# Optimization experiments

Hardware: AMD Instinct MI355X
Metric: run time of the kernel (lower is better)

Reference implementation:

```python
import jax, jax.numpy as jnp
import numpy as np

B = 2
L = 1024
D_MODEL = 1024
D_INNER = 2048   # expand * d_model
D_STATE = 16
DT_RANK = 64     # ceil(d_model / 16)
D_CONV = 4


def setup_inputs() -> dict:
    key = jax.random.key(0)
    ks = jax.random.split(key, 8)
    def nrm(k, shape, scale):
        return jax.random.normal(k, shape, dtype=jnp.float32) * scale
    A_log = jnp.log(jnp.tile(jnp.arange(1, D_STATE + 1, dtype=jnp.float32)[None, :], (D_INNER, 1)))
    return dict(
        hidden_states=jax.random.normal(ks[0], (B, L, D_MODEL), dtype=jnp.float32),
        Win=nrm(ks[1], (D_MODEL, 2 * D_INNER), D_MODEL ** -0.5),
        Wx=nrm(ks[2], (D_INNER, DT_RANK + 2 * D_STATE), D_INNER ** -0.5),
        Wdt=nrm(ks[3], (DT_RANK, D_INNER), DT_RANK ** -0.5),
        dt_bias=nrm(ks[4], (D_INNER,), 1.0),
        Wout=nrm(ks[5], (D_INNER, D_MODEL), D_INNER ** -0.5),
        dw_kernel=nrm(ks[6], (D_CONV, D_INNER), 0.2),
        dw_bias=jnp.zeros((D_INNER,), dtype=jnp.float32),
        A_log=A_log,
        Dskip=jnp.ones((D_INNER,), dtype=jnp.float32),
    )


def _causal_depthwise_conv(x, kernel, bias):
    # x: (B, L, D_INNER), kernel: (k, D_INNER); dilation 1, causal left pad
    k = kernel.shape[0]
    Lq = x.shape[1]
    xpad = jnp.pad(x, ((0, 0), (k - 1, 0), (0, 0)))
    y = sum(xpad[:, i:i + Lq, :] * kernel[i] for i in range(k)) + bias
    return jax.nn.silu(y)


def _selective_scan(u, delta, A, Bm, Cm, Dskip, z):
    # u, delta, z: (B, L, D); A: (D, N); Bm, Cm: (B, L, N)
    deltaA = jnp.exp(jnp.einsum('bld,dn->bldn', delta, A))      # (B,L,D,N)
    deltaBu = jnp.einsum('bld,bln,bld->bldn', delta, Bm, u)     # (B,L,D,N)

    def step(x_prev, elems):
        dA, dBu, c = elems                                      # (B,D,N),(B,D,N),(B,N)
        x_new = dA * x_prev + dBu
        y = jnp.einsum('bdn,bn->bd', x_new, c)
        return x_new, y

    x0 = jnp.zeros((u.shape[0], u.shape[2], A.shape[1]), dtype=jnp.float32)
    _, ys = jax.lax.scan(
        step, x0,
        (deltaA.transpose(1, 0, 2, 3), deltaBu.transpose(1, 0, 2, 3), Cm.transpose(1, 0, 2)))
    y = ys.transpose(1, 0, 2) + u * Dskip                        # skip connection
    return y * jax.nn.silu(z)


def reference(hidden_states, Win, Wx, Wdt, dt_bias, Wout, dw_kernel, dw_bias, A_log, Dskip):
    xz = hidden_states @ Win                                     # (B,L,2*D_INNER)
    x, z = jnp.split(xz, 2, axis=-1)
    A = -jnp.exp(A_log)                                          # (D_INNER, D_STATE)
    x = _causal_depthwise_conv(x, dw_kernel, dw_bias)
    x_dbl = x @ Wx                                               # (B,L,DT_RANK+2*N)
    dt, Bm, Cm = jnp.split(x_dbl, [DT_RANK, DT_RANK + D_STATE], axis=-1)
    delta = jax.nn.softplus(dt @ Wdt + dt_bias)                  # delta_bias + softplus
    y = _selective_scan(x, delta, A, Bm, Cm, Dskip, z)
    return y @ Wout
```

## Files before the change

kernel.cpp:

```cpp
#include <hip/hip_runtime.h>
#include <hip/hip_bf16.h>
#include <math.h>

#define B_SZ 2
#define L_SZ 1024
#define DM 1024
#define DI 2048
#define NS 16
#define DTR 64
#define NCHUNK 16
#define CLEN 64
#define XDLD 128
#define KSPLIT 8

typedef unsigned short ushortT;
typedef __attribute__((ext_vector_type(8))) short short8;
typedef __attribute__((ext_vector_type(4))) float floatx4;

__device__ __forceinline__ ushortT f2bf(float f) {
  unsigned u = __float_as_uint(f);
  unsigned r = (u + 0x7fff + ((u >> 16) & 1)) >> 16;
  return (ushortT)r;
}

__device__ __forceinline__ void gl2lds16(const void* g, void* l) {
  __builtin_amdgcn_global_load_lds(
      (const __attribute__((address_space(1))) unsigned int*)g,
      (__attribute__((address_space(3))) unsigned int*)l, 16, 0, 0);
}

__device__ __forceinline__ unsigned stash_addr(unsigned i) {
  return (i >> 10) * 4096 + 1024 + (i & 1023);
}

__global__ __launch_bounds__(256) void cvt_bf16(const float* __restrict__ src,
                                                ushortT* __restrict__ dst) {
  const int i = blockIdx.x * 256 + threadIdx.x;
  float4 v = ((const float4*)src)[i];
  unsigned lo = (unsigned)f2bf(v.x) | ((unsigned)f2bf(v.y) << 16);
  unsigned hi = (unsigned)f2bf(v.z) | ((unsigned)f2bf(v.w) << 16);
  ((uint2*)dst)[i] = make_uint2(lo, hi);
}

__global__ __launch_bounds__(256) void transpose_bf16(
    const float* __restrict__ src, ushortT* __restrict__ dst, int R, int C) {
  __shared__ float t[32][33];
  const int bx = blockIdx.x * 32;
  const int by = blockIdx.y * 32;
  const int tx = threadIdx.x, ty = threadIdx.y;
#pragma unroll
  for (int j = 0; j < 4; ++j)
    t[ty + j * 8][tx] = src[(size_t)(by + ty + j * 8) * C + bx + tx];
  __syncthreads();
#pragma unroll
  for (int j = 0; j < 4; ++j)
    dst[(size_t)(bx + ty + j * 8) * R + by + tx] = f2bf(t[tx][ty + j * 8]);
}

__global__ __launch_bounds__(256) void wx_pad_t(const float* __restrict__ Wx,
                                                ushortT* __restrict__ WxT) {
  const int k = blockIdx.x * 256 + threadIdx.x;
  const int n = blockIdx.y;
  WxT[(size_t)n * DI + k] = (n < 96) ? f2bf(Wx[(size_t)k * 96 + n]) : (ushortT)0;
}

__global__ __launch_bounds__(128) void gemm1_bk64(
    const ushortT* __restrict__ A, int lda,
    const ushortT* __restrict__ BT, int ldb,
    float* __restrict__ C, int ldc, int K) {
  __shared__ __align__(16) char smem[128 * 128 + 64 * 128];
  char* As = smem;
  char* Bs = smem + 128 * 128;
  const int tid = threadIdx.x;
  const int lane = tid & 63;
  const int quad = lane >> 4;
  const int l16 = lane & 15;
  const int wm = tid >> 6;
  const int m0 = blockIdx.y * 128;
  const int n0 = blockIdx.x * 64;

  floatx4 acc[4][4] = {};

  for (int k0 = 0; k0 < K; k0 += 64) {
    for (int i = tid; i < 128 * 8; i += 128) {
      const int r = i >> 3, c = i & 7;
      const int cg = c ^ (r & 7);
      gl2lds16(A + (size_t)(m0 + r) * lda + k0 + cg * 8, As + (i - lane) * 16);
    }
    for (int i = tid; i < 64 * 8; i += 128) {
      const int r = i >> 3, c = i & 7;
      const int cg = c ^ (r & 7);
      gl2lds16(BT + (size_t)(n0 + r) * ldb + k0 + cg * 8, Bs + (i - lane) * 16);
    }
    __syncthreads();

    short8 afr[4][2], bfr[4][2];
#pragma unroll
    for (int i = 0; i < 4; ++i) {
      const int r = wm * 64 + i * 16 + l16;
#pragma unroll
      for (int s = 0; s < 2; ++s)
        afr[i][s] = *(const short8*)(As + r * 128 + (((s * 4 + quad) ^ (r & 7)) * 16));
    }
#pragma unroll
    for (int j = 0; j < 4; ++j) {
      const int r = j * 16 + l16;
#pragma unroll
      for (int s = 0; s < 2; ++s)
        bfr[j][s] = *(const short8*)(Bs + r * 128 + (((s * 4 + quad) ^ (r & 7)) * 16));
    }
#pragma unroll
    for (int s = 0; s < 2; ++s)
#pragma unroll
      for (int i = 0; i < 4; ++i)
#pragma unroll
        for (int j = 0; j < 4; ++j)
          acc[i][j] = __builtin_amdgcn_mfma_f32_16x16x32_bf16(afr[i][s], bfr[j][s],
                                                              acc[i][j], 0, 0, 0);
    __syncthreads();
  }
#pragma unroll
  for (int i = 0; i < 4; ++i)
#pragma unroll
    for (int j = 0; j < 4; ++j)
#pragma unroll
      for (int r = 0; r < 4; ++r) {
        const int m = m0 + wm * 64 + i * 16 + quad * 4 + r;
        const int n = n0 + j * 16 + l16;
        C[(size_t)m * ldc + n] = acc[i][j][r];
      }
}

__global__ __launch_bounds__(128) void gemm_out_split(
    const ushortT* __restrict__ A, int lda,
    const ushortT* __restrict__ BT, int ldb,
    float* __restrict__ part) {
  __shared__ __align__(16) char smem[64 * 128 + 64 * 128];
  char* As = smem;
  char* Bs = smem + 64 * 128;
  const int tid = threadIdx.x;
  const int lane = tid & 63;
  const int quad = lane >> 4;
  const int l16 = lane & 15;
  const int wm = tid >> 6;
  const int m0 = blockIdx.y * 64;
  const int n0 = blockIdx.x * 64;
  const int kb = blockIdx.z * (DI / 2);

  floatx4 acc[2][4] = {};

  for (int k0 = kb; k0 < kb + DI / 2; k0 += 64) {
    for (int i = tid; i < 64 * 8; i += 128) {
      const int r = i >> 3, c = i & 7;
      const int cg = c ^ (r & 7);
      gl2lds16(A + (size_t)(m0 + r) * lda + k0 + cg * 8, As + (i - lane) * 16);
    }
    for (int i = tid; i < 64 * 8; i += 128) {
      const int r = i >> 3, c = i & 7;
      const int cg = c ^ (r & 7);
      gl2lds16(BT + (size_t)(n0 + r) * ldb + k0 + cg * 8, Bs + (i - lane) * 16);
    }
    __syncthreads();

    short8 afr[2][2], bfr[4][2];
#pragma unroll
    for (int i = 0; i < 2; ++i) {
      const int m = wm * 32 + i * 16 + l16;
#pragma unroll
      for (int s = 0; s < 2; ++s)
        afr[i][s] = *(const short8*)(As + m * 128 + (((s * 4 + quad) ^ (m & 7)) * 16));
    }
#pragma unroll
    for (int j = 0; j < 4; ++j) {
      const int n = j * 16 + l16;
#pragma unroll
      for (int s = 0; s < 2; ++s)
        bfr[j][s] = *(const short8*)(Bs + n * 128 + (((s * 4 + quad) ^ (n & 7)) * 16));
    }
#pragma unroll
    for (int s = 0; s < 2; ++s)
#pragma unroll
      for (int i = 0; i < 2; ++i)
#pragma unroll
        for (int j = 0; j < 4; ++j)
          acc[i][j] = __builtin_amdgcn_mfma_f32_16x16x32_bf16(afr[i][s], bfr[j][s],
                                                              acc[i][j], 0, 0, 0);
    __syncthreads();
  }
  float* out = part + (size_t)blockIdx.z * (B_SZ * L_SZ * DM);
#pragma unroll
  for (int i = 0; i < 2; ++i)
#pragma unroll
    for (int j = 0; j < 4; ++j)
#pragma unroll
      for (int r = 0; r < 4; ++r) {
        const int m = m0 + wm * 32 + i * 16 + quad * 4 + r;
        const int n = n0 + j * 16 + l16;
        out[(size_t)m * DM + n] = acc[i][j][r];
      }
}

__global__ __launch_bounds__(256) void reduce_out(const float* __restrict__ part,
                                                  float* __restrict__ out) {
  const int i = blockIdx.x * 256 + threadIdx.x;
  const float4 a = ((const float4*)part)[i];
  const float4 b = ((const float4*)part)[(size_t)(B_SZ * L_SZ * DM / 4) + i];
  ((float4*)out)[i] = make_float4(a.x + b.x, a.y + b.y, a.z + b.z, a.w + b.w);
}

__global__ __launch_bounds__(256) void gemm_xdbl_mfma(
    const float* __restrict__ xc, const ushortT* __restrict__ WxT,
    float* __restrict__ part) {
  __shared__ __align__(16) char smem[64 * 128 + 128 * 64];
  char* As = smem;
  char* Bs = smem + 64 * 128;
  const int tid = threadIdx.x;
  const int lane = tid & 63;
  const int quad = lane >> 4;
  const int l16 = lane & 15;
  const int wid = tid >> 6;
  const int wm = wid & 1;
  const int wn = wid >> 1;
  const int m0 = blockIdx.x * 64;
  const int kbase = blockIdx.y * (DI / KSPLIT);

  floatx4 acc[2][4] = {};

  for (int kk = 0; kk < DI / KSPLIT; kk += 32) {
    const int k0 = kbase + kk;
    for (int i = tid; i < 64 * 8; i += 256) {
      const int r = i >> 3, c = i & 7;
      const int cg = c ^ (r & 7);
      gl2lds16(xc + (size_t)(m0 + r) * DI + k0 + cg * 4, As + (i - lane) * 16);
    }
    for (int i = tid; i < 128 * 4; i += 256) {
      const int r = i >> 2, c = i & 3;
      const int cg = c ^ (r & 3);
      gl2lds16(WxT + (size_t)r * DI + k0 + cg * 8, Bs + (i - lane) * 16);
    }
    __syncthreads();

    short8 afr[2], bfr[4];
#pragma unroll
    for (int i = 0; i < 2; ++i) {
      const int m = wm * 32 + i * 16 + l16;
      const float4 x0 = *(const float4*)(As + m * 128 + (((quad * 2 + 0) ^ (m & 7)) * 16));
      const float4 x1 = *(const float4*)(As + m * 128 + (((quad * 2 + 1) ^ (m & 7)) * 16));
      short8 f;
      f[0] = (short)f2bf(x0.x); f[1] = (short)f2bf(x0.y);
      f[2] = (short)f2bf(x0.z); f[3] = (short)f2bf(x0.w);
      f[4] = (short)f2bf(x1.x); f[5] = (short)f2bf(x1.y);
      f[6] = (short)f2bf(x1.z); f[7] = (short)f2bf(x1.w);
      afr[i] = f;
    }
#pragma unroll
    for (int j = 0; j < 4; ++j) {
      const int n = wn * 64 + j * 16 + l16;
      bfr[j] = *(const short8*)(Bs + n * 64 + ((quad ^ (n & 3)) * 16));
    }
#pragma unroll
    for (int i = 0; i < 2; ++i)
#pragma unroll
      for (int j = 0; j < 4; ++j)
        acc[i][j] = __builtin_amdgcn_mfma_f32_16x16x32_bf16(afr[i], bfr[j],
                                                            acc[i][j], 0, 0, 0);
    __syncthreads();
  }
  float* out = part + (size_t)blockIdx.y * (B_SZ * L_SZ * XDLD);
#pragma unroll
  for (int i = 0; i < 2; ++i)
#pragma unroll
    for (int j = 0; j < 4; ++j)
#pragma unroll
      for (int r = 0; r < 4; ++r) {
        const int m = m0 + wm * 32 + i * 16 + quad * 4 + r;
        const int n = wn * 64 + j * 16 + l16;
        out[(size_t)m * XDLD + n] = acc[i][j][r];
      }
}

__global__ __launch_bounds__(256) void xdbl_reduce(const float* __restrict__ part,
                                                   float* __restrict__ xdbl) {
  const int i = blockIdx.x * 256 + threadIdx.x;
  float4 a = ((const float4*)part)[i];
#pragma unroll
  for (int s = 1; s < KSPLIT; ++s) {
    const float4 b = ((const float4*)part)[(size_t)s * (B_SZ * L_SZ * XDLD / 4) + i];
    a.x += b.x; a.y += b.y; a.z += b.z; a.w += b.w;
  }
  ((float4*)xdbl)[i] = a;
}

__global__ __launch_bounds__(256) void conv_silu(
    const float* __restrict__ xz, const float* __restrict__ kern,
    const float* __restrict__ bias, float* __restrict__ xc) {
  const int d = blockIdx.y * 256 + threadIdx.x;
  const int b = blockIdx.x >> 7;
  const int l0 = (blockIdx.x & 127) * 8;
  const int row0 = b * L_SZ + l0;
  const float k0v = kern[0 * DI + d], k1v = kern[1 * DI + d];
  const float k2v = kern[2 * DI + d], k3v = kern[3 * DI + d];
  float xv[11];
#pragma unroll
  for (int i = 0; i < 11; ++i) {
    const int l = l0 - 3 + i;
    xv[i] = (l >= 0) ? xz[((size_t)(b * L_SZ + l)) * 4096 + d] : 0.f;
  }
  const float bs = bias[d];
#pragma unroll
  for (int j = 0; j < 8; ++j) {
    float a = bs;
    a = fmaf(xv[j], k0v, a);
    a = fmaf(xv[j + 1], k1v, a);
    a = fmaf(xv[j + 2], k2v, a);
    a = fmaf(xv[j + 3], k3v, a);
    xc[(size_t)(row0 + j) * DI + d] = a / (1.f + __expf(-a));
  }
}

__global__ __launch_bounds__(256) void gemm_delta_mfma(
    const float* __restrict__ xdbl, const ushortT* __restrict__ WdtT,
    const float* __restrict__ dt_bias, float* __restrict__ delta) {
  __shared__ __align__(16) char smem[64 * 128 + 128 * 64];
  char* As = smem;
  char* Bs = smem + 64 * 128;
  const int tid = threadIdx.x;
  const int lane = tid & 63;
  const int quad = lane >> 4;
  const int l16 = lane & 15;
  const int wid = tid >> 6;
  const int wm = wid & 1;
  const int wn = wid >> 1;
  const int m0 = blockIdx.x * 64;
  const int nb0 = blockIdx.y * 128;

  floatx4 acc[2][4] = {};

#pragma unroll
  for (int k0 = 0; k0 < DTR; k0 += 32) {
    for (int i = tid; i < 64 * 8; i += 256) {
      const int r = i >> 3, c = i & 7;
      const int cg = c ^ (r & 7);
      gl2lds16(xdbl + (size_t)(m0 + r) * XDLD + k0 + cg * 4, As + (i - lane) * 16);
    }
    for (int i = tid; i < 128 * 4; i += 256) {
      const int r = i >> 2, c = i & 3;
      const int cg = c ^ (r & 3);
      gl2lds16(WdtT + (size_t)(nb0 + r) * DTR + k0 + cg * 8, Bs + (i - lane) * 16);
    }
    __syncthreads();

    short8 afr[2], bfr[4];
#pragma unroll
    for (int i = 0; i < 2; ++i) {
      const int m = wm * 32 + i * 16 + l16;
      const float4 x0 = *(const float4*)(As + m * 128 + (((quad * 2 + 0) ^ (m & 7)) * 16));
      const float4 x1 = *(const float4*)(As + m * 128 + (((quad * 2 + 1) ^ (m & 7)) * 16));
      short8 f;
      f[0] = (short)f2bf(x0.x); f[1] = (short)f2bf(x0.y);
      f[2] = (short)f2bf(x0.z); f[3] = (short)f2bf(x0.w);
      f[4] = (short)f2bf(x1.x); f[5] = (short)f2bf(x1.y);
      f[6] = (short)f2bf(x1.z); f[7] = (short)f2bf(x1.w);
      afr[i] = f;
    }
#pragma unroll
    for (int j = 0; j < 4; ++j) {
      const int n = wn * 64 + j * 16 + l16;
      bfr[j] = *(const short8*)(Bs + n * 64 + ((quad ^ (n & 3)) * 16));
    }
#pragma unroll
    for (int i = 0; i < 2; ++i)
#pragma unroll
      for (int j = 0; j < 4; ++j)
        acc[i][j] = __builtin_amdgcn_mfma_f32_16x16x32_bf16(afr[i], bfr[j],
                                                            acc[i][j], 0, 0, 0);
    __syncthreads();
  }
#pragma unroll
  for (int i = 0; i < 2; ++i)
#pragma unroll
    for (int j = 0; j < 4; ++j) {
      const int n = nb0 + wn * 64 + j * 16 + l16;
      const float bias = dt_bias[n];
#pragma unroll
      for (int r = 0; r < 4; ++r) {
        const int m = m0 + wm * 32 + i * 16 + quad * 4 + r;
        const float a = acc[i][j][r] + bias;
        delta[(size_t)m * DI + n] = (a > 20.f) ? a : log1pf(__expf(a));
      }
    }
}

__global__ __launch_bounds__(256) void scan_phase1(
    const float* __restrict__ delta, const float* __restrict__ xc,
    const float* __restrict__ xdbl, const float* __restrict__ A_log,
    float* __restrict__ xz) {
  const int bx = blockIdx.x;
  const int b = bx >> 9;
  const int c = (bx >> 5) & 15;
  const int dt = bx & 31;
  const int tid = threadIdx.x;
  const int dl = tid >> 2, nq = tid & 3;
  const int d = dt * 64 + dl;
  const int row0 = b * L_SZ + c * CLEN;

  __shared__ float Bsh[CLEN][16];
  for (int i = tid; i < CLEN * 16; i += 256)
    Bsh[i >> 4][i & 15] = xdbl[(size_t)(row0 + (i >> 4)) * XDLD + 64 + (i & 15)];

  float Av[4];
#pragma unroll
  for (int j = 0; j < 4; ++j) Av[j] = -__expf(A_log[d * 16 + nq * 4 + j]);
  float x[4] = {}, P[4] = {1.f, 1.f, 1.f, 1.f};
  __syncthreads();

  const float* dp = delta + (size_t)row0 * DI + d;
  const float* up = xc + (size_t)row0 * DI + d;
  float dB[4], uB[4];
#pragma unroll
  for (int j = 0; j < 4; ++j) { dB[j] = dp[(size_t)j * DI]; uB[j] = up[(size_t)j * DI]; }
  for (int l0 = 0; l0 < CLEN; l0 += 4) {
    float dN[4] = {}, uN[4] = {};
    if (l0 + 4 < CLEN) {
#pragma unroll
      for (int j = 0; j < 4; ++j) {
        dN[j] = dp[(size_t)(l0 + 4 + j) * DI];
        uN[j] = up[(size_t)(l0 + 4 + j) * DI];
      }
    }
#pragma unroll
    for (int jj = 0; jj < 4; ++jj) {
      const float dlt = dB[jj];
      const float t = dlt * uB[jj];
      const float* bb = &Bsh[l0 + jj][nq * 4];
#pragma unroll
      for (int n = 0; n < 4; ++n) {
        const float dA = __expf(dlt * Av[n]);
        P[n] *= dA;
        x[n] = fmaf(dA, x[n], t * bb[n]);
      }
    }
#pragma unroll
    for (int j = 0; j < 4; ++j) { dB[j] = dN[j]; uB[j] = uN[j]; }
  }
  const unsigned sb = ((unsigned)((b * NCHUNK + c) * DI + d)) * 16 + nq * 4;
  *(float4*)&xz[stash_addr(sb)] = make_float4(P[0], P[1], P[2], P[3]);
  *(float4*)&xz[stash_addr((1u << 20) + sb)] = make_float4(x[0], x[1], x[2], x[3]);
}

__global__ __launch_bounds__(256) void scan_phase2(float* __restrict__ xz) {
  const int t = blockIdx.x * 256 + threadIdx.x;
  const int b = t >> 15;
  const int rem = t & 32767;
  float x = 0.f;
#pragma unroll
  for (int c = 0; c < NCHUNK; ++c) {
    const unsigned i = ((unsigned)(b * NCHUNK + c) << 15) + rem;
    float* Pr = &xz[stash_addr(i)];
    float* Sr = &xz[stash_addr((1u << 20) + i)];
    const float P = *Pr, S = *Sr;
    *Sr = x;
    x = fmaf(P, x, S);
  }
}

__global__ __launch_bounds__(256) void scan_phase3(
    const float* __restrict__ delta, const float* __restrict__ xc,
    const float* __restrict__ xdbl, const float* __restrict__ A_log,
    const float* __restrict__ Dskip, float* __restrict__ xz) {
  const int bx = blockIdx.x;
  const int b = bx >> 9;
  const int c = (bx >> 5) & 15;
  const int dt = bx & 31;
  const int tid = threadIdx.x;
  const int dl = tid >> 2, nq = tid & 3;
  const int d = dt * 64 + dl;
  const int row0 = b * L_SZ + c * CLEN;

  __shared__ float Bsh[CLEN][16], Csh[CLEN][16];
  for (int i = tid; i < CLEN * 32; i += 256) {
    const int r = i >> 5, q = i & 31;
    const float v = xdbl[(size_t)(row0 + r) * XDLD + 64 + q];
    if (q < 16) Bsh[r][q] = v; else Csh[r][q - 16] = v;
  }

  float Av[4];
#pragma unroll
  for (int j = 0; j < 4; ++j) Av[j] = -__expf(A_log[d * 16 + nq * 4 + j]);
  const float Dsk = Dskip[d];
  const unsigned sb = ((unsigned)((b * NCHUNK + c) * DI + d)) * 16 + nq * 4;
  const float4 xi = *(const float4*)&xz[stash_addr((1u << 20) + sb)];
  float x[4] = {xi.x, xi.y, xi.z, xi.w};
  __syncthreads();

  const float* dp = delta + (size_t)row0 * DI + d;
  const float* up = xc + (size_t)row0 * DI + d;
  const float* zp = xz + (size_t)row0 * 4096 + DI + d;
  ushortT* yb = (ushortT*)xz;

  float dB[4], uB[4], zB[4];
#pragma unroll
  for (int j = 0; j < 4; ++j) {
    dB[j] = dp[(size_t)j * DI];
    uB[j] = up[(size_t)j * DI];
    zB[j] = zp[(size_t)j * 4096];
  }
  for (int l0 = 0; l0 < CLEN; l0 += 4) {
    float dN[4] = {}, uN[4] = {}, zN[4] = {};
    if (l0 + 4 < CLEN) {
#pragma unroll
      for (int j = 0; j < 4; ++j) {
        dN[j] = dp[(size_t)(l0 + 4 + j) * DI];
        uN[j] = up[(size_t)(l0 + 4 + j) * DI];
        zN[j] = zp[(size_t)(l0 + 4 + j) * 4096];
      }
    }
#pragma unroll
    for (int jj = 0; jj < 4; ++jj) {
      const float dlt = dB[jj];
      const float u = uB[jj];
      const float t = dlt * u;
      const float* bb = &Bsh[l0 + jj][nq * 4];
      const float* cc = &Csh[l0 + jj][nq * 4];
      float y = 0.f;
#pragma unroll
      for (int n = 0; n < 4; ++n) {
        const float dA = __expf(dlt * Av[n]);
        x[n] = fmaf(dA, x[n], t * bb[n]);
        y = fmaf(x[n], cc[n], y);
      }
      y += __shfl_xor(y, 1);
      y += __shfl_xor(y, 2);
      if (nq == 0) {
        const float z = zB[jj];
        const float g = (y + u * Dsk) * (z / (1.f + __expf(-z)));
        yb[(size_t)(row0 + l0 + jj) * 8192 + d] = f2bf(g);
      }
    }
#pragma unroll
    for (int j = 0; j < 4; ++j) { dB[j] = dN[j]; uB[j] = uN[j]; zB[j] = zN[j]; }
  }
}

extern "C" void kernel_launch(void* const* d_in, const int* in_sizes, int n_in,
                              void* d_out, int out_size, void* d_ws, size_t ws_size,
                              hipStream_t stream) {
  const float* hidden  = (const float*)d_in[0];
  const float* Win     = (const float*)d_in[1];
  const float* Wx      = (const float*)d_in[2];
  const float* Wdt     = (const float*)d_in[3];
  const float* dt_bias = (const float*)d_in[4];
  const float* Wout    = (const float*)d_in[5];
  const float* dwk     = (const float*)d_in[6];
  const float* dwb     = (const float*)d_in[7];
  const float* A_log   = (const float*)d_in[8];
  const float* Dskip   = (const float*)d_in[9];

  char* ws = (char*)d_ws;
  float* xz       = (float*)ws;
  float* shared16 = (float*)(ws + (32u << 20));
  float* xc       = (float*)(ws + (48u << 20));
  char* dob = (char*)d_out;
  ushortT* hidb = (ushortT*)dob;
  float* xdbl   = (float*)(dob + (4u << 20));
  ushortT* WxT  = (ushortT*)(dob + (5u << 20));
  ushortT* WdtT = (ushortT*)(dob + (5u << 20) + (512u << 10));

  cvt_bf16<<<dim3(B_SZ * L_SZ * DM / 1024), 256, 0, stream>>>(hidden, hidb);
  transpose_bf16<<<dim3(4096 / 32, 1024 / 32), dim3(32, 8), 0, stream>>>(
      Win, (ushortT*)shared16, DM, 2 * DI);
  wx_pad_t<<<dim3(DI / 256, 128), 256, 0, stream>>>(Wx, WxT);
  transpose_bf16<<<dim3(DI / 32, DTR / 32), dim3(32, 8), 0, stream>>>(
      Wdt, WdtT, DTR, DI);
  gemm1_bk64<<<dim3(4096 / 64, 2048 / 128), 128, 0, stream>>>(
      hidb, DM, (ushortT*)shared16, DM, xz, 2 * DI, DM);
  conv_silu<<<dim3(B_SZ * L_SZ / 8, DI / 256), 256, 0, stream>>>(xz, dwk, dwb, xc);
  gemm_xdbl_mfma<<<dim3(B_SZ * L_SZ / 64, KSPLIT), 256, 0, stream>>>(
      xc, WxT, shared16);
  xdbl_reduce<<<dim3(B_SZ * L_SZ * XDLD / 1024), 256, 0, stream>>>(shared16, xdbl);
  gemm_delta_mfma<<<dim3(B_SZ * L_SZ / 64, DI / 128), 256, 0, stream>>>(
      xdbl, WdtT, dt_bias, shared16);
  scan_phase1<<<dim3(B_SZ * NCHUNK * (DI / 64)), 256, 0, stream>>>(
      shared16, xc, xdbl, A_log, xz);
  scan_phase2<<<dim3(B_SZ * DI * NS / 256), 256, 0, stream>>>(xz);
  scan_phase3<<<dim3(B_SZ * NCHUNK * (DI / 64)), 256, 0, stream>>>(
      shared16, xc, xdbl, A_log, Dskip, xz);
  transpose_bf16<<<dim3(1024 / 32, 2048 / 32), dim3(32, 8), 0, stream>>>(
      Wout, (ushortT*)shared16, DI, DM);
  gemm_out_split<<<dim3(1024 / 64, 2048 / 64, 2), 128, 0, stream>>>(
      (ushortT*)xz, 4 * DI, (ushortT*)shared16, DI, xc);
  reduce_out<<<dim3(B_SZ * L_SZ * DM / 1024), 256, 0, stream>>>(xc, (float*)d_out);
}
```

Baseline: 256.2 us.

## Store conv output in bf16 and enlarge first GEMM tile to 128x128

```diff
diff --git a/kernel.cpp b/kernel.cpp
--- a/kernel.cpp
+++ b/kernel.cpp
@@ -23,6 +23,10 @@
   return (ushortT)r;
 }
 
+__device__ __forceinline__ float bf2f(ushortT v) {
+  return __uint_as_float((unsigned)v << 16);
+}
+
 __device__ __forceinline__ void gl2lds16(const void* g, void* l) {
   __builtin_amdgcn_global_load_lds(
       (const __attribute__((address_space(1))) unsigned int*)g,
@@ -64,30 +68,32 @@
   WxT[(size_t)n * DI + k] = (n < 96) ? f2bf(Wx[(size_t)k * 96 + n]) : (ushortT)0;
 }
 
-__global__ __launch_bounds__(128) void gemm1_bk64(
+__global__ __launch_bounds__(256) void gemm1_big(
     const ushortT* __restrict__ A, int lda,
     const ushortT* __restrict__ BT, int ldb,
     float* __restrict__ C, int ldc, int K) {
-  __shared__ __align__(16) char smem[128 * 128 + 64 * 128];
+  __shared__ __align__(16) char smem[128 * 128 + 128 * 128];
   char* As = smem;
   char* Bs = smem + 128 * 128;
   const int tid = threadIdx.x;
   const int lane = tid & 63;
   const int quad = lane >> 4;
   const int l16 = lane & 15;
-  const int wm = tid >> 6;
+  const int wid = tid >> 6;
+  const int wm = wid & 1;
+  const int wn = wid >> 1;
   const int m0 = blockIdx.y * 128;
-  const int n0 = blockIdx.x * 64;
+  const int n0 = blockIdx.x * 128;
 
   floatx4 acc[4][4] = {};
 
   for (int k0 = 0; k0 < K; k0 += 64) {
-    for (int i = tid; i < 128 * 8; i += 128) {
+    for (int i = tid; i < 128 * 8; i += 256) {
       const int r = i >> 3, c = i & 7;
       const int cg = c ^ (r & 7);
       gl2lds16(A + (size_t)(m0 + r) * lda + k0 + cg * 8, As + (i - lane) * 16);
     }
-    for (int i = tid; i < 64 * 8; i += 128) {
+    for (int i = tid; i < 128 * 8; i += 256) {
       const int r = i >> 3, c = i & 7;
       const int cg = c ^ (r & 7);
       gl2lds16(BT + (size_t)(n0 + r) * ldb + k0 + cg * 8, Bs + (i - lane) * 16);
@@ -104,7 +110,7 @@
     }
 #pragma unroll
     for (int j = 0; j < 4; ++j) {
-      const int r = j * 16 + l16;
+      const int r = wn * 64 + j * 16 + l16;
 #pragma unroll
       for (int s = 0; s < 2; ++s)
         bfr[j][s] = *(const short8*)(Bs + r * 128 + (((s * 4 + quad) ^ (r & 7)) * 16));
@@ -126,7 +132,7 @@
 #pragma unroll
       for (int r = 0; r < 4; ++r) {
         const int m = m0 + wm * 64 + i * 16 + quad * 4 + r;
-        const int n = n0 + j * 16 + l16;
+        const int n = n0 + wn * 64 + j * 16 + l16;
         C[(size_t)m * ldc + n] = acc[i][j][r];
       }
 }
@@ -209,11 +215,11 @@
 }
 
 __global__ __launch_bounds__(256) void gemm_xdbl_mfma(
-    const float* __restrict__ xc, const ushortT* __restrict__ WxT,
+    const ushortT* __restrict__ xcb, const ushortT* __restrict__ WxT,
     float* __restrict__ part) {
-  __shared__ __align__(16) char smem[64 * 128 + 128 * 64];
+  __shared__ __align__(16) char smem[64 * 64 + 128 * 64];
   char* As = smem;
-  char* Bs = smem + 64 * 128;
+  char* Bs = smem + 64 * 64;
   const int tid = threadIdx.x;
   const int lane = tid & 63;
   const int quad = lane >> 4;
@@ -228,10 +234,10 @@
 
   for (int kk = 0; kk < DI / KSPLIT; kk += 32) {
     const int k0 = kbase + kk;
-    for (int i = tid; i < 64 * 8; i += 256) {
-      const int r = i >> 3, c = i & 7;
-      const int cg = c ^ (r & 7);
-      gl2lds16(xc + (size_t)(m0 + r) * DI + k0 + cg * 4, As + (i - lane) * 16);
+    for (int i = tid; i < 64 * 4; i += 256) {
+      const int r = i >> 2, c = i & 3;
+      const int cg = c ^ (r & 3);
+      gl2lds16(xcb + (size_t)(m0 + r) * DI + k0 + cg * 8, As + (i - lane) * 16);
     }
     for (int i = tid; i < 128 * 4; i += 256) {
       const int r = i >> 2, c = i & 3;
@@ -244,14 +250,7 @@
 #pragma unroll
     for (int i = 0; i < 2; ++i) {
       const int m = wm * 32 + i * 16 + l16;
-      const float4 x0 = *(const float4*)(As + m * 128 + (((quad * 2 + 0) ^ (m & 7)) * 16));
-      const float4 x1 = *(const float4*)(As + m * 128 + (((quad * 2 + 1) ^ (m & 7)) * 16));
-      short8 f;
-      f[0] = (short)f2bf(x0.x); f[1] = (short)f2bf(x0.y);
-      f[2] = (short)f2bf(x0.z); f[3] = (short)f2bf(x0.w);
-      f[4] = (short)f2bf(x1.x); f[5] = (short)f2bf(x1.y);
-      f[6] = (short)f2bf(x1.z); f[7] = (short)f2bf(x1.w);
-      afr[i] = f;
+      afr[i] = *(const short8*)(As + m * 64 + ((quad ^ (m & 3)) * 16));
     }
 #pragma unroll
     for (int j = 0; j < 4; ++j) {
@@ -293,7 +292,7 @@
 
 __global__ __launch_bounds__(256) void conv_silu(
     const float* __restrict__ xz, const float* __restrict__ kern,
-    const float* __restrict__ bias, float* __restrict__ xc) {
+    const float* __restrict__ bias, ushortT* __restrict__ xcb) {
   const int d = blockIdx.y * 256 + threadIdx.x;
   const int b = blockIdx.x >> 7;
   const int l0 = (blockIdx.x & 127) * 8;
@@ -314,7 +313,7 @@
     a = fmaf(xv[j + 1], k1v, a);
     a = fmaf(xv[j + 2], k2v, a);
     a = fmaf(xv[j + 3], k3v, a);
-    xc[(size_t)(row0 + j) * DI + d] = a / (1.f + __expf(-a));
+    xcb[(size_t)(row0 + j) * DI + d] = f2bf(a / (1.f + __expf(-a)));
   }
 }
 
@@ -392,7 +391,7 @@
 }
 
 __global__ __launch_bounds__(256) void scan_phase1(
-    const float* __restrict__ delta, const float* __restrict__ xc,
+    const float* __restrict__ delta, const ushortT* __restrict__ xcb,
     const float* __restrict__ xdbl, const float* __restrict__ A_log,
     float* __restrict__ xz) {
   const int bx = blockIdx.x;
@@ -415,17 +414,20 @@
   __syncthreads();
 
   const float* dp = delta + (size_t)row0 * DI + d;
-  const float* up = xc + (size_t)row0 * DI + d;
+  const ushortT* up = xcb + (size_t)row0 * DI + d;
   float dB[4], uB[4];
 #pragma unroll
-  for (int j = 0; j < 4; ++j) { dB[j] = dp[(size_t)j * DI]; uB[j] = up[(size_t)j * DI]; }
+  for (int j = 0; j < 4; ++j) {
+    dB[j] = dp[(size_t)j * DI];
+    uB[j] = bf2f(up[(size_t)j * DI]);
+  }
   for (int l0 = 0; l0 < CLEN; l0 += 4) {
     float dN[4] = {}, uN[4] = {};
     if (l0 + 4 < CLEN) {
 #pragma unroll
       for (int j = 0; j < 4; ++j) {
         dN[j] = dp[(size_t)(l0 + 4 + j) * DI];
-        uN[j] = up[(size_t)(l0 + 4 + j) * DI];
+        uN[j] = bf2f(up[(size_t)(l0 + 4 + j) * DI]);
       }
     }
 #pragma unroll
@@ -465,7 +467,7 @@
 }
 
 __global__ __launch_bounds__(256) void scan_phase3(
-    const float* __restrict__ delta, const float* __restrict__ xc,
+    const float* __restrict__ delta, const ushortT* __restrict__ xcb,
     const float* __restrict__ xdbl, const float* __restrict__ A_log,
     const float* __restrict__ Dskip, float* __restrict__ xz) {
   const int bx = blockIdx.x;
@@ -494,7 +496,7 @@
   __syncthreads();
 
   const float* dp = delta + (size_t)row0 * DI + d;
-  const float* up = xc + (size_t)row0 * DI + d;
+  const ushortT* up = xcb + (size_t)row0 * DI + d;
   const float* zp = xz + (size_t)row0 * 4096 + DI + d;
   ushortT* yb = (ushortT*)xz;
 
@@ -502,7 +504,7 @@
 #pragma unroll
   for (int j = 0; j < 4; ++j) {
     dB[j] = dp[(size_t)j * DI];
-    uB[j] = up[(size_t)j * DI];
+    uB[j] = bf2f(up[(size_t)j * DI]);
     zB[j] = zp[(size_t)j * 4096];
   }
   for (int l0 = 0; l0 < CLEN; l0 += 4) {
@@ -511,7 +513,7 @@
 #pragma unroll
       for (int j = 0; j < 4; ++j) {
         dN[j] = dp[(size_t)(l0 + 4 + j) * DI];
-        uN[j] = up[(size_t)(l0 + 4 + j) * DI];
+        uN[j] = bf2f(up[(size_t)(l0 + 4 + j) * DI]);
         zN[j] = zp[(size_t)(l0 + 4 + j) * 4096];
       }
     }
@@ -559,7 +561,8 @@
   char* ws = (char*)d_ws;
   float* xz       = (float*)ws;
   float* shared16 = (float*)(ws + (32u << 20));
-  float* xc       = (float*)(ws + (48u << 20));
+  float* xcreg    = (float*)(ws + (48u << 20));
+  ushortT* xcb    = (ushortT*)xcreg;
   char* dob = (char*)d_out;
   ushortT* hidb = (ushortT*)dob;
   float* xdbl   = (float*)(dob + (4u << 20));
@@ -572,22 +575,22 @@
   wx_pad_t<<<dim3(DI / 256, 128), 256, 0, stream>>>(Wx, WxT);
   transpose_bf16<<<dim3(DI / 32, DTR / 32), dim3(32, 8), 0, stream>>>(
       Wdt, WdtT, DTR, DI);
-  gemm1_bk64<<<dim3(4096 / 64, 2048 / 128), 128, 0, stream>>>(
+  gemm1_big<<<dim3(4096 / 128, 2048 / 128), 256, 0, stream>>>(
       hidb, DM, (ushortT*)shared16, DM, xz, 2 * DI, DM);
-  conv_silu<<<dim3(B_SZ * L_SZ / 8, DI / 256), 256, 0, stream>>>(xz, dwk, dwb, xc);
+  conv_silu<<<dim3(B_SZ * L_SZ / 8, DI / 256), 256, 0, stream>>>(xz, dwk, dwb, xcb);
   gemm_xdbl_mfma<<<dim3(B_SZ * L_SZ / 64, KSPLIT), 256, 0, stream>>>(
-      xc, WxT, shared16);
+      xcb, WxT, shared16);
   xdbl_reduce<<<dim3(B_SZ * L_SZ * XDLD / 1024), 256, 0, stream>>>(shared16, xdbl);
   gemm_delta_mfma<<<dim3(B_SZ * L_SZ / 64, DI / 128), 256, 0, stream>>>(
       xdbl, WdtT, dt_bias, shared16);
   scan_phase1<<<dim3(B_SZ * NCHUNK * (DI / 64)), 256, 0, stream>>>(
-      shared16, xc, xdbl, A_log, xz);
+      shared16, xcb, xdbl, A_log, xz);
   scan_phase2<<<dim3(B_SZ * DI * NS / 256), 256, 0, stream>>>(xz);
   scan_phase3<<<dim3(B_SZ * NCHUNK * (DI / 64)), 256, 0, stream>>>(
-      shared16, xc, xdbl, A_log, Dskip, xz);
+      shared16, xcb, xdbl, A_log, Dskip, xz);
   transpose_bf16<<<dim3(1024 / 32, 2048 / 32), dim3(32, 8), 0, stream>>>(
       Wout, (ushortT*)shared16, DI, DM);
   gemm_out_split<<<dim3(1024 / 64, 2048 / 64, 2), 128, 0, stream>>>(
-      (ushortT*)xz, 4 * DI, (ushortT*)shared16, DI, xc);
-  reduce_out<<<dim3(B_SZ * L_SZ * DM / 1024), 256, 0, stream>>>(xc, (float*)d_out);
-}
+      (ushortT*)xz, 4 * DI, (ushortT*)shared16, DI, xcreg);
+  reduce_out<<<dim3(B_SZ * L_SZ * DM / 1024), 256, 0, stream>>>(xcreg, (float*)d_out);
+}
```

Result: no change. 254.0 us (-0.9%).
